# Kernel tuning notes

Measured on AMD Instinct MI355X. Metric: run time of the kernel, lower is better.

The kernel has to match this reference:

```python
import jax, jax.numpy as jnp
import numpy as np

B, S, HID = 2, 2048, 2048
H, KV, D = 16, 8, 128
EPS = 1e-6


def _rope_embeds(B, S, D):
    # standard RoPE cos/sin table, concatenated along last dim: [B, S, D]
    pos = jnp.arange(S, dtype=jnp.float32)  # same positions per batch row
    inv_freq = 1.0 / (10000.0 ** (jnp.arange(0, D // 2, dtype=jnp.float32) * (2.0 / D)))
    ang = pos[:, None] * inv_freq[None, :]  # [S, D/2]
    pe = jnp.concatenate([jnp.cos(ang), jnp.sin(ang)], axis=-1)  # [S, D]
    return jnp.broadcast_to(pe[None], (B, S, D))


def setup_inputs() -> dict:
    key = jax.random.key(0)
    ks = jax.random.split(key, 5)
    scale = 0.02
    return {
        "x": jax.random.normal(ks[0], (B, S, HID), jnp.float32),
        "pos_embeds": _rope_embeds(B, S, D),
        "q_w": jax.random.normal(ks[1], (H * D, HID), jnp.float32) * scale,
        "k_w": jax.random.normal(ks[2], (KV * D, HID), jnp.float32) * scale,
        "v_w": jax.random.normal(ks[3], (KV * D, HID), jnp.float32) * scale,
        "o_w": jax.random.normal(ks[4], (HID, H * D), jnp.float32) * scale,
        "q_norm_w": jnp.ones((D,), jnp.float32),
        "k_norm_w": jnp.ones((D,), jnp.float32),
    }


def _rmsnorm(x, w):
    var = jnp.mean(jnp.square(x), axis=-1, keepdims=True)
    return x * jax.lax.rsqrt(var + EPS) * w


def _apply_rope(x, pos_embeds):
    # x: [B, S, h, D]; pos_embeds: [B, S, D] = cat(cos, sin)
    x1, x2 = jnp.split(x, 2, axis=-1)
    cos, sin = jnp.split(pos_embeds[:, :, None, :], 2, axis=-1)
    return jnp.concatenate([x1 * cos - x2 * sin, x1 * sin + x2 * cos], axis=-1)


def reference(x, pos_embeds, q_w, k_w, v_w, o_w, q_norm_w, k_norm_w):
    b, s, _ = x.shape
    q = _apply_rope(_rmsnorm((x @ q_w.T).reshape(b, s, H, D), q_norm_w), pos_embeds)
    k = _apply_rope(_rmsnorm((x @ k_w.T).reshape(b, s, KV, D), k_norm_w), pos_embeds)
    v = (x @ v_w.T).reshape(b, s, KV, D)
    # GQA: repeat kv heads to match query heads
    rep = H // KV
    k = jnp.repeat(k, rep, axis=2)
    v = jnp.repeat(v, rep, axis=2)
    scores = jnp.einsum("bqhd,bkhd->bhqk", q, k) * (1.0 / np.sqrt(D))
    causal = jnp.tril(jnp.ones((s, s), dtype=bool))
    scores = jnp.where(causal[None, None], scores, jnp.finfo(scores.dtype).min)
    attn = jax.nn.softmax(scores, axis=-1)
    out = jnp.einsum("bhqk,bkhd->bqhd", attn, v).reshape(b, s, H * D)
    return out @ o_w.T
```

## Files before the change

### kernel.cpp

```cpp
#include <hip/hip_runtime.h>
#include <hip/hip_bf16.h>

#define BATCH 2
#define SEQ   2048
#define HID   2048
#define NH    16
#define NKV   8
#define HD    128

typedef __bf16 bf16;
typedef bf16  bf16x8  __attribute__((ext_vector_type(8)));
typedef bf16  bf16x4  __attribute__((ext_vector_type(4)));
typedef float floatx4 __attribute__((ext_vector_type(4)));

typedef __attribute__((address_space(3))) void lds_void;
typedef const __attribute__((address_space(1))) void gmem_void;

__device__ inline void async16(const void* g, void* l) {
    __builtin_amdgcn_global_load_lds((gmem_void*)g, (lds_void*)l, 16, 0, 0);
}

#define XN  8388608u
#define QWN 4194304u
#define KWN 2097152u
#define VWN 2097152u
#define OWN 4194304u

__global__ __launch_bounds__(256) void cvt_all(bf16* __restrict__ dst,
                                               const float* __restrict__ x,
                                               const float* __restrict__ qw,
                                               const float* __restrict__ kw,
                                               const float* __restrict__ vw,
                                               const float* __restrict__ ow)
{
    const int blk = blockIdx.x;
    const float* src;
    size_t off;
    if (blk < 4096)      { src = x;  off = (size_t)blk * 2048; }
    else if (blk < 6144) { src = qw; off = (size_t)(blk - 4096) * 2048; }
    else if (blk < 7168) { src = kw; off = (size_t)(blk - 6144) * 2048; }
    else if (blk < 8192) { src = vw; off = (size_t)(blk - 7168) * 2048; }
    else                 { src = ow; off = (size_t)(blk - 8192) * 2048; }

    const int t = threadIdx.x * 8;
    const float4* p = (const float4*)(src + off + t);
    float4 u0 = p[0], u1 = p[1];
    bf16x8 v;
    v[0] = (bf16)u0.x; v[1] = (bf16)u0.y; v[2] = (bf16)u0.z; v[3] = (bf16)u0.w;
    v[4] = (bf16)u1.x; v[5] = (bf16)u1.y; v[6] = (bf16)u1.z; v[7] = (bf16)u1.w;
    *(bf16x8*)(dst + (size_t)blk * 2048 + t) = v;
}

template <int AMODE, int WMODE, int CMODE>
__global__ __launch_bounds__(256) void gemm128(void* __restrict__ Cp,
                                               const void* __restrict__ Ap,
                                               const void* __restrict__ Wp,
                                               int M, int N, int K)
{
    __shared__ bf16 As[128 * 64];
    __shared__ bf16 Ws[128 * 64];

    const int tid  = threadIdx.x;
    const int wv   = tid >> 6;
    const int lane = tid & 63;
    const int quad = lane >> 4;
    const int c    = lane & 15;

    const int m0 = blockIdx.x * 128;
    const int n0 = blockIdx.y * 128;
    const int wm = (wv >> 1) * 64;
    const int wn = (wv & 1) * 64;

    const int arow = lane >> 3;
    const int acol = (lane & 7) * 8;

    floatx4 acc[4][4] = {};

    for (int k0 = 0; k0 < K; k0 += 64) {
        if constexpr (AMODE == 0) {
            const float* A = (const float*)Ap;
            #pragma unroll
            for (int it = 0; it < 4; it++) {
                int row = it * 32 + (tid >> 3);
                int col = (tid & 7) * 8;
                const float4* p = (const float4*)(A + (size_t)(m0 + row) * K + k0 + col);
                float4 u0 = p[0], u1 = p[1];
                bf16x8 v;
                v[0] = (bf16)u0.x; v[1] = (bf16)u0.y; v[2] = (bf16)u0.z; v[3] = (bf16)u0.w;
                v[4] = (bf16)u1.x; v[5] = (bf16)u1.y; v[6] = (bf16)u1.z; v[7] = (bf16)u1.w;
                *(bf16x8*)(&As[row * 64 + col]) = v;
            }
        } else {
            const bf16* A = (const bf16*)Ap;
            #pragma unroll
            for (int ch = 0; ch < 4; ch++) {
                int row = wv * 32 + ch * 8 + arow;
                async16(A + (size_t)(m0 + row) * K + k0 + acol,
                        &As[(wv * 32 + ch * 8) * 64]);
            }
        }
        if constexpr (WMODE == 0) {
            const float* W = (const float*)Wp;
            #pragma unroll
            for (int it = 0; it < 4; it++) {
                int row = it * 32 + (tid >> 3);
                int col = (tid & 7) * 8;
                const float4* p = (const float4*)(W + (size_t)(n0 + row) * K + k0 + col);
                float4 u0 = p[0], u1 = p[1];
                bf16x8 v;
                v[0] = (bf16)u0.x; v[1] = (bf16)u0.y; v[2] = (bf16)u0.z; v[3] = (bf16)u0.w;
                v[4] = (bf16)u1.x; v[5] = (bf16)u1.y; v[6] = (bf16)u1.z; v[7] = (bf16)u1.w;
                *(bf16x8*)(&Ws[row * 64 + col]) = v;
            }
        } else {
            const bf16* W = (const bf16*)Wp;
            #pragma unroll
            for (int ch = 0; ch < 4; ch++) {
                int row = wv * 32 + ch * 8 + arow;
                async16(W + (size_t)(n0 + row) * K + k0 + acol,
                        &Ws[(wv * 32 + ch * 8) * 64]);
            }
        }
        __syncthreads();

        #pragma unroll
        for (int t = 0; t < 2; t++) {
            bf16x8 af[4], bw[4];
            #pragma unroll
            for (int i = 0; i < 4; i++)
                af[i] = *(const bf16x8*)(&As[(wm + i * 16 + c) * 64 + t * 32 + quad * 8]);
            #pragma unroll
            for (int j = 0; j < 4; j++)
                bw[j] = *(const bf16x8*)(&Ws[(wn + j * 16 + c) * 64 + t * 32 + quad * 8]);
            #pragma unroll
            for (int i = 0; i < 4; i++)
                #pragma unroll
                for (int j = 0; j < 4; j++)
                    acc[i][j] = __builtin_amdgcn_mfma_f32_16x16x32_bf16(af[i], bw[j], acc[i][j], 0, 0, 0);
        }
        __syncthreads();
    }

    if constexpr (CMODE == 0) {
        float* C = (float*)Cp;
        #pragma unroll
        for (int i = 0; i < 4; i++)
            #pragma unroll
            for (int j = 0; j < 4; j++)
                #pragma unroll
                for (int r = 0; r < 4; r++) {
                    int m = m0 + wm + i * 16 + quad * 4 + r;
                    int n = n0 + wn + j * 16 + c;
                    C[(size_t)m * N + n] = acc[i][j][r];
                }
    } else if constexpr (CMODE == 1) {
        bf16* C = (bf16*)Cp;
        #pragma unroll
        for (int i = 0; i < 4; i++)
            #pragma unroll
            for (int j = 0; j < 4; j++)
                #pragma unroll
                for (int r = 0; r < 4; r++) {
                    int m = m0 + wm + i * 16 + quad * 4 + r;
                    int n = n0 + wn + j * 16 + c;
                    C[(size_t)m * N + n] = (bf16)acc[i][j][r];
                }
    } else if constexpr (CMODE == 2) {
        bf16* C = (bf16*)Cp;
        const int b = m0 >> 11;
        #pragma unroll
        for (int j = 0; j < 4; j++) {
            int n = n0 + wn + j * 16 + c;
            size_t base = ((size_t)b * N + n) * 2048;
            #pragma unroll
            for (int i = 0; i < 4; i++) {
                int s0 = (m0 & 2047) + wm + i * 16 + quad * 4;
                bf16x4 v;
                #pragma unroll
                for (int r = 0; r < 4; r++) v[r] = (bf16)acc[i][j][r];
                *(bf16x4*)(&C[base + s0]) = v;
            }
        }
    } else {
        bf16* Cq = (bf16*)Cp;
        if (n0 < 2048) {
            #pragma unroll
            for (int i = 0; i < 4; i++)
                #pragma unroll
                for (int j = 0; j < 4; j++)
                    #pragma unroll
                    for (int r = 0; r < 4; r++) {
                        int m = m0 + wm + i * 16 + quad * 4 + r;
                        int n = n0 + wn + j * 16 + c;
                        Cq[(size_t)m * 2048 + n] = (bf16)acc[i][j][r];
                    }
        } else if (n0 < 3072) {
            bf16* Ck = Cq + XN;
            #pragma unroll
            for (int i = 0; i < 4; i++)
                #pragma unroll
                for (int j = 0; j < 4; j++)
                    #pragma unroll
                    for (int r = 0; r < 4; r++) {
                        int m = m0 + wm + i * 16 + quad * 4 + r;
                        int n = n0 - 2048 + wn + j * 16 + c;
                        Ck[(size_t)m * 1024 + n] = (bf16)acc[i][j][r];
                    }
        } else {
            bf16* Cv = Cq + XN + QWN;
            const int b = m0 >> 11;
            #pragma unroll
            for (int j = 0; j < 4; j++) {
                int n = n0 - 3072 + wn + j * 16 + c;
                size_t base = ((size_t)b * 1024 + n) * 2048;
                #pragma unroll
                for (int i = 0; i < 4; i++) {
                    int s0 = (m0 & 2047) + wm + i * 16 + quad * 4;
                    bf16x4 v;
                    #pragma unroll
                    for (int r = 0; r < 4; r++) v[r] = (bf16)acc[i][j][r];
                    *(bf16x4*)(&Cv[base + s0]) = v;
                }
            }
        }
    }
}

__global__ __launch_bounds__(256) void gemm_o64(float* __restrict__ C,
                                                const bf16* __restrict__ A,
                                                const bf16* __restrict__ W,
                                                int M, int N, int K)
{
    __shared__ bf16 As[128 * 64];
    __shared__ bf16 Ws[64 * 64];

    const int tid  = threadIdx.x;
    const int wv   = tid >> 6;
    const int lane = tid & 63;
    const int quad = lane >> 4;
    const int c    = lane & 15;

    const int m0 = blockIdx.x * 128;
    const int n0 = blockIdx.y * 64;
    const int wm = (wv >> 1) * 64;
    const int wn = (wv & 1) * 32;

    const int arow = lane >> 3;
    const int acol = (lane & 7) * 8;

    floatx4 acc[4][2] = {};

    for (int k0 = 0; k0 < K; k0 += 64) {
        #pragma unroll
        for (int ch = 0; ch < 4; ch++) {
            int row = wv * 32 + ch * 8 + arow;
            async16(A + (size_t)(m0 + row) * K + k0 + acol,
                    &As[(wv * 32 + ch * 8) * 64]);
        }
        #pragma unroll
        for (int ch = 0; ch < 2; ch++) {
            int row = wv * 16 + ch * 8 + arow;
            async16(W + (size_t)(n0 + row) * K + k0 + acol,
                    &Ws[(wv * 16 + ch * 8) * 64]);
        }
        __syncthreads();

        #pragma unroll
        for (int t = 0; t < 2; t++) {
            bf16x8 af[4], bw[2];
            #pragma unroll
            for (int i = 0; i < 4; i++)
                af[i] = *(const bf16x8*)(&As[(wm + i * 16 + c) * 64 + t * 32 + quad * 8]);
            #pragma unroll
            for (int j = 0; j < 2; j++)
                bw[j] = *(const bf16x8*)(&Ws[(wn + j * 16 + c) * 64 + t * 32 + quad * 8]);
            #pragma unroll
            for (int i = 0; i < 4; i++)
                #pragma unroll
                for (int j = 0; j < 2; j++)
                    acc[i][j] = __builtin_amdgcn_mfma_f32_16x16x32_bf16(af[i], bw[j], acc[i][j], 0, 0, 0);
        }
        __syncthreads();
    }

    #pragma unroll
    for (int i = 0; i < 4; i++)
        #pragma unroll
        for (int j = 0; j < 2; j++)
            #pragma unroll
            for (int r = 0; r < 4; r++) {
                int m = m0 + wm + i * 16 + quad * 4 + r;
                int n = n0 + wn + j * 16 + c;
                C[(size_t)m * N + n] = acc[i][j][r];
            }
}

__global__ __launch_bounds__(128) void norm_rope_k(bf16* __restrict__ k,
                                                   const float* __restrict__ pe,
                                                   const float* __restrict__ knw)
{
    const int s  = blockIdx.x;
    const int hh = blockIdx.y;
    const int b  = blockIdx.z;
    const int d  = threadIdx.x;

    bf16* buf = k + (size_t)(b * SEQ + s) * 1024 + hh * HD;

    float x = (float)buf[d];
    float ss = x * x;
    #pragma unroll
    for (int m = 32; m; m >>= 1) ss += __shfl_xor(ss, m);

    __shared__ float red[2];
    __shared__ float nv[128];
    if ((d & 63) == 0) red[d >> 6] = ss;
    __syncthreads();
    float var = (red[0] + red[1]) * (1.0f / 128.0f);
    float nx = x * rsqrtf(var + 1e-6f) * knw[d];
    nv[d] = nx;
    __syncthreads();

    const float* pev = pe + ((size_t)b * SEQ + s) * HD;
    float o;
    if (d < 64) {
        o = nx * pev[d] - nv[d + 64] * pev[64 + d];
    } else {
        o = nv[d - 64] * pev[d] + nx * pev[d - 64];
    }
    buf[d] = (bf16)o;
}

__global__ __launch_bounds__(256) void fattn(bf16* __restrict__ O,
                                             const bf16* __restrict__ Q,
                                             const bf16* __restrict__ Kh,
                                             const bf16* __restrict__ Vtg,
                                             const float* __restrict__ pe,
                                             const float* __restrict__ qnw)
{
    const int h    = blockIdx.y;
    const int b    = blockIdx.z;
    const int qblk = (h & 8) ? (int)blockIdx.x
                             : ((int)gridDim.x - 1 - (int)blockIdx.x);
    const int kv   = h >> 1;

    const int tid  = threadIdx.x;
    const int wv   = tid >> 6;
    const int lane = tid & 63;
    const int quad = lane >> 4;
    const int c    = lane & 15;

    __shared__ bf16 Ks[64 * 136];
    __shared__ bf16 Vs[128 * 72];

    const int qw = qblk * 64 + wv * 16;

    bf16x8 qf[4];
    {
        const bf16* qp = Q + (size_t)(b * SEQ + qw + c) * 2048 + h * HD + quad * 8;
        float qv[4][8];
        float ss = 0.0f;
        #pragma unroll
        for (int t = 0; t < 4; t++) {
            bf16x8 raw = *(const bf16x8*)(qp + t * 32);
            #pragma unroll
            for (int j = 0; j < 8; j++) { qv[t][j] = (float)raw[j]; ss += qv[t][j] * qv[t][j]; }
        }
        ss += __shfl_xor(ss, 16);
        ss += __shfl_xor(ss, 32);
        const float inv = rsqrtf(ss * (1.0f / 128.0f) + 1e-6f);
        const float* pev = pe + (size_t)(b * SEQ + qw + c) * HD + quad * 8;
        float nx[4][8], pv[4][8];
        #pragma unroll
        for (int t = 0; t < 4; t++)
            #pragma unroll
            for (int j = 0; j < 8; j++) {
                pv[t][j] = pev[t * 32 + j];
                nx[t][j] = qv[t][j] * inv * qnw[t * 32 + quad * 8 + j];
            }
        #pragma unroll
        for (int t = 0; t < 2; t++)
            #pragma unroll
            for (int j = 0; j < 8; j++) {
                qf[t][j]     = (bf16)(nx[t][j] * pv[t][j]     - nx[t + 2][j] * pv[t + 2][j]);
                qf[t + 2][j] = (bf16)(nx[t][j] * pv[t + 2][j] + nx[t + 2][j] * pv[t][j]);
            }
    }

    floatx4 o_acc[8] = {};
    float l_part[4] = {};

    const bf16* kbase = Kh  + (size_t)b * SEQ * 1024 + kv * HD;
    const bf16* vbase = Vtg + ((size_t)b * 1024 + kv * HD) * 2048;

    const int kr  = tid >> 2, ksc = (tid & 3) * 32;
    const int vd  = tid >> 1, vkc = (tid & 1) * 32;
    bf16* psw = &Ks[wv * 16 * 72];
    const int nkt = qblk + 1;
    const float kS = 0.08838834764831845f * 1.4426950408889634f;
    const float kB = 11.5f * 1.4426950408889634f;

    bf16x8 kreg[4], vreg[4];
    {
        const bf16* kp = kbase + (size_t)kr * 1024 + ksc;
        const bf16* vp = vbase + (size_t)vd * 2048 + vkc;
        #pragma unroll
        for (int i = 0; i < 4; i++) kreg[i] = *(const bf16x8*)(kp + i * 8);
        #pragma unroll
        for (int i = 0; i < 4; i++) vreg[i] = *(const bf16x8*)(vp + i * 8);
    }

    for (int kt = 0; kt < nkt; kt++) {
        const int k0 = kt * 64;
        #pragma unroll
        for (int i = 0; i < 4; i++)
            *(bf16x8*)(&Ks[kr * 136 + ksc + i * 8]) = kreg[i];
        #pragma unroll
        for (int i = 0; i < 4; i++)
            *(bf16x8*)(&Vs[vd * 72 + vkc + i * 8]) = vreg[i];
        __syncthreads();

        if (kt + 1 < nkt) {
            const bf16* kp = kbase + (size_t)(k0 + 64 + kr) * 1024 + ksc;
            const bf16* vp = vbase + (size_t)vd * 2048 + (k0 + 64) + vkc;
            #pragma unroll
            for (int i = 0; i < 4; i++) kreg[i] = *(const bf16x8*)(kp + i * 8);
            #pragma unroll
            for (int i = 0; i < 4; i++) vreg[i] = *(const bf16x8*)(vp + i * 8);
        }

        floatx4 sc[4] = {};
        #pragma unroll
        for (int t = 0; t < 4; t++) {
            #pragma unroll
            for (int g = 0; g < 4; g++) {
                bf16x8 kf = *(const bf16x8*)(&Ks[(g * 16 + c) * 136 + t * 32 + quad * 8]);
                sc[g] = __builtin_amdgcn_mfma_f32_16x16x32_bf16(qf[t], kf, sc[g], 0, 0, 0);
            }
        }

        asm volatile("" ::: "memory");
        __builtin_amdgcn_s_barrier();
        asm volatile("" ::: "memory");

        const bool last = (kt == nkt - 1);
        #pragma unroll
        for (int r = 0; r < 4; r++) {
            const int qrow = qw + quad * 4 + r;
            #pragma unroll
            for (int g = 0; g < 4; g++) {
                float p = exp2f(sc[g][r] * kS - kB);
                if (last && (k0 + g * 16 + c > qrow)) p = 0.0f;
                l_part[r] += p;
                psw[(quad * 4 + r) * 72 + g * 16 + c] = (bf16)p;
            }
        }
        asm volatile("s_waitcnt lgkmcnt(0)" ::: "memory");
        bf16x8 pf0 = *(const bf16x8*)(&psw[c * 72 + quad * 8]);
        bf16x8 pf1 = *(const bf16x8*)(&psw[c * 72 + 32 + quad * 8]);

        #pragma unroll
        for (int f = 0; f < 8; f++) {
            bf16x8 vf0 = *(const bf16x8*)(&Vs[(f * 16 + c) * 72 + quad * 8]);
            bf16x8 vf1 = *(const bf16x8*)(&Vs[(f * 16 + c) * 72 + 32 + quad * 8]);
            o_acc[f] = __builtin_amdgcn_mfma_f32_16x16x32_bf16(pf0, vf0, o_acc[f], 0, 0, 0);
            o_acc[f] = __builtin_amdgcn_mfma_f32_16x16x32_bf16(pf1, vf1, o_acc[f], 0, 0, 0);
        }
        __syncthreads();
    }

    #pragma unroll
    for (int r = 0; r < 4; r++) {
        float l = l_part[r];
        #pragma unroll
        for (int msk = 8; msk; msk >>= 1) l += __shfl_xor(l, msk);
        const float inv = 1.0f / l;
        bf16* op = O + (size_t)(b * SEQ + qw + quad * 4 + r) * 2048 + h * HD;
        #pragma unroll
        for (int f = 0; f < 8; f++) op[f * 16 + c] = (bf16)(o_acc[f][r] * inv);
    }
}

extern "C" void kernel_launch(void* const* d_in, const int* in_sizes, int n_in,
                              void* d_out, int out_size, void* d_ws, size_t ws_size,
                              hipStream_t stream)
{
    const float* x   = (const float*)d_in[0];
    const float* pe  = (const float*)d_in[1];
    const float* qw  = (const float*)d_in[2];
    const float* kw  = (const float*)d_in[3];
    const float* vw  = (const float*)d_in[4];
    const float* ow  = (const float*)d_in[5];
    const float* qnw = (const float*)d_in[6];
    const float* knw = (const float*)d_in[7];
    float* out = (float*)d_out;

    bf16* qb = (bf16*)d_ws;
    bf16* kb = qb + XN;
    bf16* vt = kb + KWN * 2;
    bf16* ab = vt + VWN * 2;
    bf16* cvt_base = ab + XN;

    const bool fit = ws_size >= (size_t)92274688;
    const int M = BATCH * SEQ;

    if (fit) {
        bf16* xb  = cvt_base;
        bf16* qwb = xb  + XN;
        bf16* owb = qwb + QWN + KWN + VWN;

        cvt_all<<<10240, 256, 0, stream>>>(xb, x, qw, kw, vw, ow);

        gemm128<1, 1, 3><<<dim3(32, 32), 256, 0, stream>>>(qb, xb, qwb, M, 4096, 2048);

        norm_rope_k<<<dim3(SEQ, NKV, BATCH), 128, 0, stream>>>(kb, pe, knw);
        fattn<<<dim3(SEQ / 64, NH, BATCH), 256, 0, stream>>>(ab, qb, kb, vt, pe, qnw);

        gemm_o64<<<dim3(32, 32), 256, 0, stream>>>(out, ab, owb, M, 2048, 2048);
    } else {
        gemm128<0, 0, 1><<<dim3(32, 16), 256, 0, stream>>>(qb, x, qw, M, 2048, 2048);
        gemm128<0, 0, 1><<<dim3(32,  8), 256, 0, stream>>>(kb, x, kw, M, 1024, 2048);
        gemm128<0, 0, 2><<<dim3(32,  8), 256, 0, stream>>>(vt, x, vw, M, 1024, 2048);

        norm_rope_k<<<dim3(SEQ, NKV, BATCH), 128, 0, stream>>>(kb, pe, knw);
        fattn<<<dim3(SEQ / 64, NH, BATCH), 256, 0, stream>>>(ab, qb, kb, vt, pe, qnw);

        gemm128<0, 0, 0><<<dim3(32, 16), 256, 0, stream>>>(out, ab, ow, M, 2048, 2048);
    }
}
```

Before: 401.6 us.

## Double attention query tile to 128 rows with 8 waves and reuse gemm128 for O-proj

The flash attention kernel now uses 512 threads per block and covers 128 query rows, so each loaded K/V tile is shared by twice as many waves. Per-thread staging loads are halved. Waves whose rows lie entirely above the causal diagonal skip the MMA and softmax work, and the mask is applied on the last two tiles. The dedicated 128x64 output-projection GEMM is dropped in favour of the generic 128x128 gemm128 kernel. The trade-off is half as many attention blocks, which worsens the causal load imbalance across blocks.

Result: no change. 398.1 us (-0.9%).

```diff
diff --git a/kernel.cpp b/kernel.cpp
--- a/kernel.cpp
+++ b/kernel.cpp
@@ -226,75 +226,6 @@
     }
 }
 
-__global__ __launch_bounds__(256) void gemm_o64(float* __restrict__ C,
-                                                const bf16* __restrict__ A,
-                                                const bf16* __restrict__ W,
-                                                int M, int N, int K)
-{
-    __shared__ bf16 As[128 * 64];
-    __shared__ bf16 Ws[64 * 64];
-
-    const int tid  = threadIdx.x;
-    const int wv   = tid >> 6;
-    const int lane = tid & 63;
-    const int quad = lane >> 4;
-    const int c    = lane & 15;
-
-    const int m0 = blockIdx.x * 128;
-    const int n0 = blockIdx.y * 64;
-    const int wm = (wv >> 1) * 64;
-    const int wn = (wv & 1) * 32;
-
-    const int arow = lane >> 3;
-    const int acol = (lane & 7) * 8;
-
-    floatx4 acc[4][2] = {};
-
-    for (int k0 = 0; k0 < K; k0 += 64) {
-        #pragma unroll
-        for (int ch = 0; ch < 4; ch++) {
-            int row = wv * 32 + ch * 8 + arow;
-            async16(A + (size_t)(m0 + row) * K + k0 + acol,
-                    &As[(wv * 32 + ch * 8) * 64]);
-        }
-        #pragma unroll
-        for (int ch = 0; ch < 2; ch++) {
-            int row = wv * 16 + ch * 8 + arow;
-            async16(W + (size_t)(n0 + row) * K + k0 + acol,
-                    &Ws[(wv * 16 + ch * 8) * 64]);
-        }
-        __syncthreads();
-
-        #pragma unroll
-        for (int t = 0; t < 2; t++) {
-            bf16x8 af[4], bw[2];
-            #pragma unroll
-            for (int i = 0; i < 4; i++)
-                af[i] = *(const bf16x8*)(&As[(wm + i * 16 + c) * 64 + t * 32 + quad * 8]);
-            #pragma unroll
-            for (int j = 0; j < 2; j++)
-                bw[j] = *(const bf16x8*)(&Ws[(wn + j * 16 + c) * 64 + t * 32 + quad * 8]);
-            #pragma unroll
-            for (int i = 0; i < 4; i++)
-                #pragma unroll
-                for (int j = 0; j < 2; j++)
-                    acc[i][j] = __builtin_amdgcn_mfma_f32_16x16x32_bf16(af[i], bw[j], acc[i][j], 0, 0, 0);
-        }
-        __syncthreads();
-    }
-
-    #pragma unroll
-    for (int i = 0; i < 4; i++)
-        #pragma unroll
-        for (int j = 0; j < 2; j++)
-            #pragma unroll
-            for (int r = 0; r < 4; r++) {
-                int m = m0 + wm + i * 16 + quad * 4 + r;
-                int n = n0 + wn + j * 16 + c;
-                C[(size_t)m * N + n] = acc[i][j][r];
-            }
-}
-
 __global__ __launch_bounds__(128) void norm_rope_k(bf16* __restrict__ k,
                                                    const float* __restrict__ pe,
                                                    const float* __restrict__ knw)
@@ -330,7 +261,7 @@
     buf[d] = (bf16)o;
 }
 
-__global__ __launch_bounds__(256) void fattn(bf16* __restrict__ O,
+__global__ __launch_bounds__(512) void fattn(bf16* __restrict__ O,
                                              const bf16* __restrict__ Q,
                                              const bf16* __restrict__ Kh,
                                              const bf16* __restrict__ Vtg,
@@ -349,10 +280,10 @@
     const int quad = lane >> 4;
     const int c    = lane & 15;
 
-    __shared__ bf16 Ks[64 * 136];
+    __shared__ bf16 Ks[64 * 152];
     __shared__ bf16 Vs[128 * 72];
 
-    const int qw = qblk * 64 + wv * 16;
+    const int qw = qblk * 128 + wv * 16;
 
     bf16x8 qf[4];
     {
@@ -392,49 +323,51 @@
     const bf16* kbase = Kh  + (size_t)b * SEQ * 1024 + kv * HD;
     const bf16* vbase = Vtg + ((size_t)b * 1024 + kv * HD) * 2048;
 
-    const int kr  = tid >> 2, ksc = (tid & 3) * 32;
-    const int vd  = tid >> 1, vkc = (tid & 1) * 32;
-    bf16* psw = &Ks[wv * 16 * 72];
-    const int nkt = qblk + 1;
+    const int kr  = tid >> 3, ksc = (tid & 7) * 16;
+    const int vd  = tid >> 2, vkc = (tid & 3) * 16;
+    bf16* psw = &Ks[wv * 1152];
+    const int nkt = 2 * qblk + 2;
     const float kS = 0.08838834764831845f * 1.4426950408889634f;
     const float kB = 11.5f * 1.4426950408889634f;
 
-    bf16x8 kreg[4], vreg[4];
+    bf16x8 kreg[2], vreg[2];
     {
         const bf16* kp = kbase + (size_t)kr * 1024 + ksc;
         const bf16* vp = vbase + (size_t)vd * 2048 + vkc;
-        #pragma unroll
-        for (int i = 0; i < 4; i++) kreg[i] = *(const bf16x8*)(kp + i * 8);
-        #pragma unroll
-        for (int i = 0; i < 4; i++) vreg[i] = *(const bf16x8*)(vp + i * 8);
+        kreg[0] = *(const bf16x8*)(kp);
+        kreg[1] = *(const bf16x8*)(kp + 8);
+        vreg[0] = *(const bf16x8*)(vp);
+        vreg[1] = *(const bf16x8*)(vp + 8);
     }
 
     for (int kt = 0; kt < nkt; kt++) {
         const int k0 = kt * 64;
-        #pragma unroll
-        for (int i = 0; i < 4; i++)
-            *(bf16x8*)(&Ks[kr * 136 + ksc + i * 8]) = kreg[i];
-        #pragma unroll
-        for (int i = 0; i < 4; i++)
-            *(bf16x8*)(&Vs[vd * 72 + vkc + i * 8]) = vreg[i];
+        *(bf16x8*)(&Ks[kr * 152 + ksc])     = kreg[0];
+        *(bf16x8*)(&Ks[kr * 152 + ksc + 8]) = kreg[1];
+        *(bf16x8*)(&Vs[vd * 72 + vkc])      = vreg[0];
+        *(bf16x8*)(&Vs[vd * 72 + vkc + 8])  = vreg[1];
         __syncthreads();
 
         if (kt + 1 < nkt) {
             const bf16* kp = kbase + (size_t)(k0 + 64 + kr) * 1024 + ksc;
             const bf16* vp = vbase + (size_t)vd * 2048 + (k0 + 64) + vkc;
-            #pragma unroll
-            for (int i = 0; i < 4; i++) kreg[i] = *(const bf16x8*)(kp + i * 8);
-            #pragma unroll
-            for (int i = 0; i < 4; i++) vreg[i] = *(const bf16x8*)(vp + i * 8);
-        }
+            kreg[0] = *(const bf16x8*)(kp);
+            kreg[1] = *(const bf16x8*)(kp + 8);
+            vreg[0] = *(const bf16x8*)(vp);
+            vreg[1] = *(const bf16x8*)(vp + 8);
+        }
+
+        const bool active = (k0 <= qw + 15);
 
         floatx4 sc[4] = {};
-        #pragma unroll
-        for (int t = 0; t < 4; t++) {
-            #pragma unroll
-            for (int g = 0; g < 4; g++) {
-                bf16x8 kf = *(const bf16x8*)(&Ks[(g * 16 + c) * 136 + t * 32 + quad * 8]);
-                sc[g] = __builtin_amdgcn_mfma_f32_16x16x32_bf16(qf[t], kf, sc[g], 0, 0, 0);
+        if (active) {
+            #pragma unroll
+            for (int t = 0; t < 4; t++) {
+                #pragma unroll
+                for (int g = 0; g < 4; g++) {
+                    bf16x8 kf = *(const bf16x8*)(&Ks[(g * 16 + c) * 152 + t * 32 + quad * 8]);
+                    sc[g] = __builtin_amdgcn_mfma_f32_16x16x32_bf16(qf[t], kf, sc[g], 0, 0, 0);
+                }
             }
         }
 
@@ -442,28 +375,30 @@
         __builtin_amdgcn_s_barrier();
         asm volatile("" ::: "memory");
 
-        const bool last = (kt == nkt - 1);
-        #pragma unroll
-        for (int r = 0; r < 4; r++) {
-            const int qrow = qw + quad * 4 + r;
-            #pragma unroll
-            for (int g = 0; g < 4; g++) {
-                float p = exp2f(sc[g][r] * kS - kB);
-                if (last && (k0 + g * 16 + c > qrow)) p = 0.0f;
-                l_part[r] += p;
-                psw[(quad * 4 + r) * 72 + g * 16 + c] = (bf16)p;
-            }
-        }
-        asm volatile("s_waitcnt lgkmcnt(0)" ::: "memory");
-        bf16x8 pf0 = *(const bf16x8*)(&psw[c * 72 + quad * 8]);
-        bf16x8 pf1 = *(const bf16x8*)(&psw[c * 72 + 32 + quad * 8]);
-
-        #pragma unroll
-        for (int f = 0; f < 8; f++) {
-            bf16x8 vf0 = *(const bf16x8*)(&Vs[(f * 16 + c) * 72 + quad * 8]);
-            bf16x8 vf1 = *(const bf16x8*)(&Vs[(f * 16 + c) * 72 + 32 + quad * 8]);
-            o_acc[f] = __builtin_amdgcn_mfma_f32_16x16x32_bf16(pf0, vf0, o_acc[f], 0, 0, 0);
-            o_acc[f] = __builtin_amdgcn_mfma_f32_16x16x32_bf16(pf1, vf1, o_acc[f], 0, 0, 0);
+        if (active) {
+            const bool tail = (kt >= nkt - 2);
+            #pragma unroll
+            for (int r = 0; r < 4; r++) {
+                const int qrow = qw + quad * 4 + r;
+                #pragma unroll
+                for (int g = 0; g < 4; g++) {
+                    float p = exp2f(sc[g][r] * kS - kB);
+                    if (tail && (k0 + g * 16 + c > qrow)) p = 0.0f;
+                    l_part[r] += p;
+                    psw[(quad * 4 + r) * 72 + g * 16 + c] = (bf16)p;
+                }
+            }
+            asm volatile("s_waitcnt lgkmcnt(0)" ::: "memory");
+            bf16x8 pf0 = *(const bf16x8*)(&psw[c * 72 + quad * 8]);
+            bf16x8 pf1 = *(const bf16x8*)(&psw[c * 72 + 32 + quad * 8]);
+
+            #pragma unroll
+            for (int f = 0; f < 8; f++) {
+                bf16x8 vf0 = *(const bf16x8*)(&Vs[(f * 16 + c) * 72 + quad * 8]);
+                bf16x8 vf1 = *(const bf16x8*)(&Vs[(f * 16 + c) * 72 + 32 + quad * 8]);
+                o_acc[f] = __builtin_amdgcn_mfma_f32_16x16x32_bf16(pf0, vf0, o_acc[f], 0, 0, 0);
+                o_acc[f] = __builtin_amdgcn_mfma_f32_16x16x32_bf16(pf1, vf1, o_acc[f], 0, 0, 0);
+            }
         }
         __syncthreads();
     }
@@ -513,16 +448,16 @@
         gemm128<1, 1, 3><<<dim3(32, 32), 256, 0, stream>>>(qb, xb, qwb, M, 4096, 2048);
 
         norm_rope_k<<<dim3(SEQ, NKV, BATCH), 128, 0, stream>>>(kb, pe, knw);
-        fattn<<<dim3(SEQ / 64, NH, BATCH), 256, 0, stream>>>(ab, qb, kb, vt, pe, qnw);
-
-        gemm_o64<<<dim3(32, 32), 256, 0, stream>>>(out, ab, owb, M, 2048, 2048);
+        fattn<<<dim3(SEQ / 128, NH, BATCH), 512, 0, stream>>>(ab, qb, kb, vt, pe, qnw);
+
+        gemm128<1, 1, 0><<<dim3(32, 16), 256, 0, stream>>>(out, ab, owb, M, 2048, 2048);
     } else {
         gemm128<0, 0, 1><<<dim3(32, 16), 256, 0, stream>>>(qb, x, qw, M, 2048, 2048);
         gemm128<0, 0, 1><<<dim3(32,  8), 256, 0, stream>>>(kb, x, kw, M, 1024, 2048);
         gemm128<0, 0, 2><<<dim3(32,  8), 256, 0, stream>>>(vt, x, vw, M, 1024, 2048);
 
         norm_rope_k<<<dim3(SEQ, NKV, BATCH), 128, 0, stream>>>(kb, pe, knw);
-        fattn<<<dim3(SEQ / 64, NH, BATCH), 256, 0, stream>>>(ab, qb, kb, vt, pe, qnw);
+        fattn<<<dim3(SEQ / 128, NH, BATCH), 512, 0, stream>>>(ab, qb, kb, vt, pe, qnw);
 
         gemm128<0, 0, 0><<<dim3(32, 16), 256, 0, stream>>>(out, ab, ow, M, 2048, 2048);
     }
```
